# Performance work log

Hardware: AMD Instinct MI355X
Metric: run time of the kernel (lower is better)

Reference implementation:

```python
import jax, jax.numpy as jnp
import numpy as np
from jax import lax

DIM = 256
D_STATE = 16
SPARSITY = 0.3


def setup_inputs() -> dict:
    key = jax.random.key(0)
    ks = jax.random.split(key, 12)
    B, L, C = 16, 8192, DIM
    x = jax.random.normal(ks[0], (B, L, C), dtype=jnp.float32)
    # DyT params
    alpha = jnp.ones((1,), jnp.float32) * 0.5
    dyt_w = jnp.ones((C,), jnp.float32) + 0.02 * jax.random.normal(ks[1], (C,))
    dyt_b = 0.02 * jax.random.normal(ks[2], (C,))
    # proj_in / proj_out (torch Linear: y = x @ W.T + b)
    s = 1.0 / np.sqrt(C)
    Wi = jax.random.uniform(ks[3], (C, C), minval=-s, maxval=s)
    bi = jax.random.uniform(ks[4], (C,), minval=-s, maxval=s)
    Wo = jax.random.uniform(ks[5], (C, C), minval=-s, maxval=s)
    bo = jax.random.uniform(ks[6], (C,), minval=-s, maxval=s)
    # depthwise kernel_size=1 conv -> per-channel scale
    conv_w = jax.random.uniform(ks[7], (C,), minval=-1.0, maxval=1.0)
    # SSM params (nn.Parameter zeros in source; use small random for a meaningful test)
    A = 0.02 * jax.random.normal(ks[8], (D_STATE, D_STATE))
    Bp = 0.02 * jax.random.normal(ks[9], (1, 1, D_STATE))
    Cp = 0.02 * jax.random.normal(ks[10], (C, D_STATE))
    return {"x": x, "alpha": alpha, "dyt_w": dyt_w, "dyt_b": dyt_b,
            "Wi": Wi, "bi": bi, "conv_w": conv_w,
            "A": A, "Bp": Bp, "Cp": Cp, "Wo": Wo, "bo": bo}


def reference(x, alpha, dyt_w, dyt_b, Wi, bi, conv_w, A, Bp, Cp, Wo, bo):
    B, L, C = x.shape
    residual = x
    # DyT norm
    x_norm = jnp.tanh(alpha * x) * dyt_w + dyt_b
    # proj_in
    x_proj = x_norm @ Wi.T + bi                      # [B, L, C]
    # cosine similarity to center token, softmax over L
    center = x_proj[:, L // 2]                        # [B, C]
    eps = 1e-12
    xpn = x_proj / jnp.maximum(jnp.linalg.norm(x_proj, axis=-1, keepdims=True), eps)
    cn = center / jnp.maximum(jnp.linalg.norm(center, axis=-1, keepdims=True), eps)
    sim = jax.nn.softmax(jnp.einsum('blc,bc->bl', xpn, cn), axis=-1)  # [B, L]
    k = max(1, int(L * SPARSITY))
    _, topk_idx = lax.top_k(sim, k)                   # [B, k]
    # gather selected tokens
    x_sparse = jnp.take_along_axis(x_proj, topk_idx[:, :, None], axis=1)  # [B, k, C]
    # depthwise kernel-1 conv == per-channel scale
    x_conv = x_sparse * conv_w                        # [B, k, C]
    # SSM scan: h_{t} = h_{t-1} @ A.T + sigmoid(B) * x_t;  y_t = sum(h * sigmoid(C))
    sB = jax.nn.sigmoid(Bp)                           # [1, 1, d_state]
    sC = jax.nn.sigmoid(Cp)                           # [C, d_state]

    def step(h, xt):
        # h: [B, C, d_state], xt: [B, C]
        h = h @ A.T + sB * xt[:, :, None]
        y = jnp.sum(h * sC, axis=-1)                  # [B, C]
        return h, y

    h0 = jnp.zeros((B, C, D_STATE), x.dtype)
    _, ys = lax.scan(step, h0, jnp.swapaxes(x_conv, 0, 1))  # ys: [k, B, C]
    x_processed = jnp.swapaxes(ys, 0, 1) @ Wo.T + bo        # [B, k, C]
    # scatter back to full sequence (topk indices are unique per row)
    out = jnp.zeros_like(x).at[jnp.arange(B)[:, None], topk_idx].set(x_processed)
    return out + residual, sim
```

## Files before the change

### kernel.cpp

```cpp
#include <hip/hip_runtime.h>
#include <math.h>

#define B_ 16
#define L_ 8192
#define C_ 256
#define KTOP 2457
#define JT 20
#define M1 (B_*L_)
#define M2 (B_*KTOP)

#define XP_OFF  ((size_t)0)
#define Y_OFF   (XP_OFF + (size_t)M1*C_)
#define CN_OFF  (Y_OFF  + (size_t)M2*C_)
#define CF_OFF  (CN_OFF + (size_t)B_*C_)
#define IDX_OFF (CF_OFF + (size_t)JT*C_)
#define WIT_OFF (IDX_OFF + (size_t)M2)
#define WOT_OFF (WIT_OFF + (size_t)C_*C_)

__device__ __forceinline__ void async_copy16(const float* g, float* l) {
    __builtin_amdgcn_global_load_lds(
        (const __attribute__((address_space(1))) void*)g,
        (__attribute__((address_space(3))) void*)l, 16, 0, 0);
}

__global__ __launch_bounds__(256) void prep_kernel(
    const float* __restrict__ Wi, const float* __restrict__ Wo,
    float* __restrict__ WiT, float* __restrict__ WoT,
    const float* __restrict__ A, const float* __restrict__ Bp, const float* __restrict__ Cp,
    float* __restrict__ cf,
    const float* __restrict__ x, const float* __restrict__ bi, const float* __restrict__ alpha,
    const float* __restrict__ dw, const float* __restrict__ db, float* __restrict__ cn)
{
    __shared__ float shm[1089];
    const int bid = blockIdx.x, tid = threadIdx.x;
    if (bid < 128) {
        const int z = bid >> 6, rem = bid & 63;
        const int r0 = (rem >> 3) * 32, c0 = (rem & 7) * 32;
        const float* src = z ? Wo : Wi;
        float* dst = z ? WoT : WiT;
        float (*t)[33] = (float(*)[33])shm;
        int tx = tid & 31, ty = tid >> 5;
        #pragma unroll
        for (int r = 0; r < 4; r++)
            t[ty + r*8][tx] = src[(size_t)(r0 + ty + r*8)*C_ + c0 + tx];
        __syncthreads();
        #pragma unroll
        for (int r = 0; r < 4; r++)
            dst[(size_t)(c0 + ty + r*8)*C_ + r0 + tx] = t[tx][ty + r*8];
    } else if (bid == 128) {
        int c = tid;
        float* As = shm;
        float* v0 = shm + 256;
        As[c] = A[c];
        if (c < 16) v0[c] = 1.0f / (1.0f + expf(-Bp[c]));
        float sC[16];
        #pragma unroll
        for (int i = 0; i < 16; i++) sC[i] = 1.0f / (1.0f + expf(-Cp[c*16 + i]));
        __syncthreads();
        float v[16];
        #pragma unroll
        for (int i = 0; i < 16; i++) v[i] = v0[i];
        for (int j = 0; j < JT; j++) {
            float d = 0.f;
            #pragma unroll
            for (int i = 0; i < 16; i++) d += sC[i] * v[i];
            cf[j*C_ + c] = d;
            float nv[16];
            #pragma unroll
            for (int i = 0; i < 16; i++) {
                float s = 0.f;
                #pragma unroll
                for (int m = 0; m < 16; m++) s += As[i*16 + m] * v[m];
                nv[i] = s;
            }
            #pragma unroll
            for (int i = 0; i < 16; i++) v[i] = nv[i];
        }
    } else {
        int b = bid - 129, c = tid;
        float* xn = shm;
        float* red = shm + 256;
        float al = alpha[0];
        size_t base = ((size_t)b*L_ + L_/2)*C_;
        xn[c] = tanhf(al*x[base + c])*dw[c] + db[c];
        __syncthreads();
        float s = bi[c];
        #pragma unroll 8
        for (int k = 0; k < 256; k++) s = fmaf(xn[k], Wi[(size_t)c*C_ + k], s);
        float ss = s*s;
        #pragma unroll
        for (int off = 32; off; off >>= 1) ss += __shfl_xor(ss, off);
        if ((c & 63) == 0) red[c >> 6] = ss;
        __syncthreads();
        float tot = red[0] + red[1] + red[2] + red[3];
        float inv = 1.0f / fmaxf(sqrtf(tot), 1e-12f);
        cn[b*C_ + c] = s * inv;
    }
}

__global__ __launch_bounds__(256, 2) void gemm1_kernel(
    const float* __restrict__ x, const float* __restrict__ WiT,
    const float* __restrict__ bi, const float* __restrict__ alpha,
    const float* __restrict__ dw, const float* __restrict__ db,
    const float* __restrict__ cn, float* __restrict__ xp, float* __restrict__ e)
{
    __shared__ float As[32*132];
    __shared__ float Bs[32*256];
    const int tid = threadIdx.x;
    const int lane = tid & 63;
    const int wv = tid >> 6;
    const int tn2 = tid & 31;
    const int tm2 = tid >> 5;
    const int m0 = blockIdx.x * 128;
    const int b  = m0 >> 13;
    const float al = alpha[0];

    float acc[16][8];
    #pragma unroll
    for (int i = 0; i < 16; i++)
        #pragma unroll
        for (int j = 0; j < 8; j++) acc[i][j] = 0.f;

    for (int k0 = 0; k0 < C_; k0 += 32) {
        #pragma unroll
        for (int it = 0; it < 8; it++) {
            int br = wv + it*4;
            async_copy16(&WiT[(size_t)(k0 + br)*C_ + lane*4], &Bs[br*256]);
        }
        #pragma unroll
        for (int it = 0; it < 4; it++) {
            int i2 = tid + it*256;
            int ar = i2 >> 3;
            int ak = (i2 & 7) * 4;
            float4 v  = *(const float4*)&x[(size_t)(m0 + ar)*C_ + k0 + ak];
            float4 w4 = *(const float4*)&dw[k0 + ak];
            float4 b4 = *(const float4*)&db[k0 + ak];
            As[(ak+0)*132 + ar] = tanhf(al*v.x)*w4.x + b4.x;
            As[(ak+1)*132 + ar] = tanhf(al*v.y)*w4.y + b4.y;
            As[(ak+2)*132 + ar] = tanhf(al*v.z)*w4.z + b4.z;
            As[(ak+3)*132 + ar] = tanhf(al*v.w)*w4.w + b4.w;
        }
        __syncthreads();
        #pragma unroll 2
        for (int kk = 0; kk < 32; kk++) {
            float a[16];
            *(float4*)&a[0]  = *(const float4*)&As[kk*132 + tm2*16];
            *(float4*)&a[4]  = *(const float4*)&As[kk*132 + tm2*16 + 4];
            *(float4*)&a[8]  = *(const float4*)&As[kk*132 + tm2*16 + 8];
            *(float4*)&a[12] = *(const float4*)&As[kk*132 + tm2*16 + 12];
            float4 b0 = *(const float4*)&Bs[kk*256 + tn2*4];
            float4 b1 = *(const float4*)&Bs[kk*256 + tn2*4 + 128];
            #pragma unroll
            for (int i = 0; i < 16; i++) {
                acc[i][0] = fmaf(a[i], b0.x, acc[i][0]);
                acc[i][1] = fmaf(a[i], b0.y, acc[i][1]);
                acc[i][2] = fmaf(a[i], b0.z, acc[i][2]);
                acc[i][3] = fmaf(a[i], b0.w, acc[i][3]);
                acc[i][4] = fmaf(a[i], b1.x, acc[i][4]);
                acc[i][5] = fmaf(a[i], b1.y, acc[i][5]);
                acc[i][6] = fmaf(a[i], b1.z, acc[i][6]);
                acc[i][7] = fmaf(a[i], b1.w, acc[i][7]);
            }
        }
        __syncthreads();
    }
    float4 bi0 = *(const float4*)&bi[tn2*4];
    float4 bi1 = *(const float4*)&bi[tn2*4 + 128];
    float4 c0  = *(const float4*)&cn[b*C_ + tn2*4];
    float4 c1  = *(const float4*)&cn[b*C_ + tn2*4 + 128];
    #pragma unroll
    for (int i = 0; i < 16; i++) {
        size_t row = m0 + tm2*16 + i;
        float4 o0 = make_float4(acc[i][0]+bi0.x, acc[i][1]+bi0.y, acc[i][2]+bi0.z, acc[i][3]+bi0.w);
        float4 o1 = make_float4(acc[i][4]+bi1.x, acc[i][5]+bi1.y, acc[i][6]+bi1.z, acc[i][7]+bi1.w);
        *(float4*)&xp[row*C_ + tn2*4]       = o0;
        *(float4*)&xp[row*C_ + tn2*4 + 128] = o1;
        float dt = o0.x*c0.x + o0.y*c0.y + o0.z*c0.z + o0.w*c0.w
                 + o1.x*c1.x + o1.y*c1.y + o1.z*c1.z + o1.w*c1.w;
        float ss = o0.x*o0.x + o0.y*o0.y + o0.z*o0.z + o0.w*o0.w
                 + o1.x*o1.x + o1.y*o1.y + o1.z*o1.z + o1.w*o1.w;
        #pragma unroll
        for (int off = 16; off; off >>= 1) {
            dt += __shfl_xor(dt, off);
            ss += __shfl_xor(ss, off);
        }
        if (tn2 == 0) e[row] = dt / fmaxf(sqrtf(ss), 1e-12f);
    }
}

__global__ __launch_bounds__(1024) void softmax_kernel(
    const float* __restrict__ e, float* __restrict__ sim, unsigned long long* __restrict__ kw)
{
    __shared__ float scratch[32];
    const int b = blockIdx.x, tid = threadIdx.x;
    const int lane = tid & 63, wid = tid >> 6;
    const float* eb = e + (size_t)b*L_;
    float ev[8];
    #pragma unroll
    for (int s = 0; s < 8; s++) ev[s] = eb[tid + s*1024];
    float mx = ev[0];
    #pragma unroll
    for (int s = 1; s < 8; s++) mx = fmaxf(mx, ev[s]);
    #pragma unroll
    for (int off = 32; off; off >>= 1) mx = fmaxf(mx, __shfl_xor(mx, off));
    if (lane == 0) scratch[wid] = mx;
    __syncthreads();
    if (tid == 0) {
        float m2 = scratch[0];
        for (int i = 1; i < 16; i++) m2 = fmaxf(m2, scratch[i]);
        scratch[20] = m2;
    }
    __syncthreads();
    mx = scratch[20];
    float pv[8], sum = 0.f;
    #pragma unroll
    for (int s = 0; s < 8; s++) { pv[s] = expf(ev[s] - mx); sum += pv[s]; }
    #pragma unroll
    for (int off = 32; off; off >>= 1) sum += __shfl_xor(sum, off);
    __syncthreads();
    if (lane == 0) scratch[wid] = sum;
    __syncthreads();
    if (tid == 0) {
        float s2 = 0.f;
        for (int i = 0; i < 16; i++) s2 += scratch[i];
        scratch[21] = s2;
    }
    __syncthreads();
    float inv = 1.0f / scratch[21];
    #pragma unroll
    for (int s = 0; s < 8; s++) {
        int l = tid + s*1024;
        float sm = pv[s] * inv;
        sim[(size_t)b*L_ + l] = sm;
        kw[(size_t)b*L_ + l] =
            ((unsigned long long)__float_as_uint(sm) << 32) | (unsigned)(0xFFFFFFFFu - l);
    }
}

__global__ __launch_bounds__(256) void sort1k_kernel(unsigned long long* __restrict__ keys)
{
    __shared__ unsigned long long k[1024];
    size_t base = (size_t)blockIdx.x * 1024;
    int tid = threadIdx.x;
    #pragma unroll
    for (int s = 0; s < 4; s++) k[tid + s*256] = keys[base + tid + s*256];
    __syncthreads();
    for (int ksz = 2; ksz <= 1024; ksz <<= 1) {
        for (int j = ksz >> 1; j > 0; j >>= 1) {
            #pragma unroll
            for (int s = 0; s < 2; s++) {
                int p = tid + s*256;
                int i = ((p & ~(j-1)) << 1) | (p & (j-1));
                int ix = i | j;
                unsigned long long a = k[i], c = k[ix];
                bool desc = ((i & ksz) == 0);
                if (desc ? (a < c) : (a > c)) { k[i] = c; k[ix] = a; }
            }
            __syncthreads();
        }
    }
    #pragma unroll
    for (int s = 0; s < 4; s++) keys[base + tid + s*256] = k[tid + s*256];
}

#define MT 2048
__global__ __launch_bounds__(256) void merge_kernel(
    const unsigned long long* __restrict__ src, unsigned long long* __restrict__ dst, int run)
{
    const size_t tile = blockIdx.x;
    const size_t pairSpan = (size_t)2 * run;
    const size_t p = tile * MT / pairSpan;
    const int o = (int)(tile * MT % pairSpan);
    const unsigned long long* A  = src + p * pairSpan;
    const unsigned long long* Bv = A + run;
    unsigned long long* D = dst + p * pairSpan;

    int q0 = o + threadIdx.x * (MT/256);
    int lo = (q0 > run) ? (q0 - run) : 0;
    int hi = (q0 < run) ? q0 : run;
    while (lo < hi) {
        int mid = (lo + hi) >> 1;
        if (A[mid] >= Bv[q0 - 1 - mid]) lo = mid + 1; else hi = mid;
    }
    int a = lo, bq = q0 - lo;
    #pragma unroll
    for (int q = 0; q < MT/256; q++) {
        unsigned long long va = (a < run) ? A[a] : 0ULL;
        unsigned long long vb = (bq < run) ? Bv[bq] : 0ULL;
        bool takeA = (bq >= run) || ((a < run) && (va > vb));
        D[q0 + q] = takeA ? va : vb;
        if (takeA) a++; else bq++;
    }
}

__global__ __launch_bounds__(256) void merge_top_kernel(
    const unsigned long long* __restrict__ src, int* __restrict__ idxo)
{
    const int tile = blockIdx.x;
    const int p = tile >> 1;
    const int o = (tile & 1) * MT;
    const int run = 4096;
    const unsigned long long* A  = src + (size_t)p * L_;
    const unsigned long long* Bv = A + run;

    int q0 = o + threadIdx.x * (MT/256);
    int lo = (q0 > run) ? (q0 - run) : 0;
    int hi = (q0 < run) ? q0 : run;
    while (lo < hi) {
        int mid = (lo + hi) >> 1;
        if (A[mid] >= Bv[q0 - 1 - mid]) lo = mid + 1; else hi = mid;
    }
    int a = lo, bq = q0 - lo;
    #pragma unroll
    for (int q = 0; q < MT/256; q++) {
        unsigned long long va = (a < run) ? A[a] : 0ULL;
        unsigned long long vb = (bq < run) ? Bv[bq] : 0ULL;
        bool takeA = (bq >= run) || ((a < run) && (va > vb));
        unsigned long long v = takeA ? va : vb;
        if (q0 + q < KTOP)
            idxo[p*KTOP + q0 + q] = (int)(0xFFFFFFFFu - (unsigned)(v & 0xFFFFFFFFu));
        if (takeA) a++; else bq++;
    }
}

#define TT 32
__global__ __launch_bounds__(256) void y_kernel(const float* __restrict__ xp,
    const int* __restrict__ idx, const float* __restrict__ conv_w,
    const float* __restrict__ cf, float* __restrict__ y)
{
    __shared__ float rows[(TT + JT - 1) * C_];
    const int b = blockIdx.y;
    const int t0 = blockIdx.x * TT;
    const int tid = threadIdx.x;
    const int c4 = (tid & 63) * 4;
    const int tg = tid >> 6;
    const int* idxb = idx + b*KTOP;

    for (int s = tid; s < (TT + JT - 1) * 64; s += 256) {
        int r = s >> 6, cq = (s & 63) * 4;
        int gi = t0 - (JT - 1) + r;
        float4 v = make_float4(0.f, 0.f, 0.f, 0.f);
        if (gi >= 0 && gi < KTOP) {
            int l = idxb[gi];
            v = *(const float4*)&xp[((size_t)b*L_ + l)*C_ + cq];
        }
        *(float4*)&rows[r*C_ + cq] = v;
    }
    float4 cfr[JT];
    #pragma unroll
    for (int j = 0; j < JT; j++) cfr[j] = *(const float4*)&cf[j*C_ + c4];
    float4 cw = *(const float4*)&conv_w[c4];
    __syncthreads();

    #pragma unroll
    for (int u = 0; u < TT/4; u++) {
        int tl = tg + u*4;
        int t = t0 + tl;
        if (t < KTOP) {
            float4 acc = make_float4(0.f, 0.f, 0.f, 0.f);
            #pragma unroll
            for (int j = 0; j < JT; j++) {
                const float4 v = *(const float4*)&rows[(tl + JT - 1 - j)*C_ + c4];
                acc.x = fmaf(cfr[j].x, v.x, acc.x);
                acc.y = fmaf(cfr[j].y, v.y, acc.y);
                acc.z = fmaf(cfr[j].z, v.z, acc.z);
                acc.w = fmaf(cfr[j].w, v.w, acc.w);
            }
            acc.x *= cw.x; acc.y *= cw.y; acc.z *= cw.z; acc.w *= cw.w;
            *(float4*)&y[((size_t)b*KTOP + t)*C_ + c4] = acc;
        }
    }
}

__global__ void copy_kernel(const float4* __restrict__ src, float4* __restrict__ dst)
{
    size_t n4 = (size_t)M1*C_/4;
    for (size_t i = (size_t)blockIdx.x*blockDim.x + threadIdx.x; i < n4;
         i += (size_t)gridDim.x*blockDim.x)
        dst[i] = src[i];
}

__global__ __launch_bounds__(256, 2) void gemm2_kernel(
    const float* __restrict__ y, const float* __restrict__ WoT,
    const float* __restrict__ bo, const float* __restrict__ x,
    const int* __restrict__ idx, float* __restrict__ out0)
{
    __shared__ float As[2][32*132];
    __shared__ float Bs[2][32*128];
    const int tid = threadIdx.x;
    const int lane = tid & 63;
    const int wv = tid >> 6;
    const int tm2 = tid >> 4;
    const int tn2 = tid & 15;
    const int m0 = blockIdx.x * 128;
    const int n0 = blockIdx.y * 128;

    float acc[8][8];
    #pragma unroll
    for (int i = 0; i < 8; i++)
        #pragma unroll
        for (int j = 0; j < 8; j++) acc[i][j] = 0.f;

    float4 xa[4];
    #pragma unroll
    for (int it = 0; it < 4; it++) {
        int i2 = tid + it*256;
        int m = m0 + (i2>>3);
        xa[it] = (m < M2) ? *(const float4*)&y[(size_t)m*C_ + ((i2&7)*4)]
                          : make_float4(0.f, 0.f, 0.f, 0.f);
    }
    #pragma unroll
    for (int it = 0; it < 4; it++) {
        int brow = 2*wv + it*8;
        async_copy16(&WoT[(size_t)(brow + (lane>>5))*C_ + n0 + (lane&31)*4],
                     &Bs[0][brow*128]);
    }
    #pragma unroll
    for (int it = 0; it < 4; it++) {
        int i2 = tid + it*256;
        int ar = i2>>3, ak = (i2&7)*4;
        float4 v = xa[it];
        As[0][(ak+0)*132 + ar] = v.x;
        As[0][(ak+1)*132 + ar] = v.y;
        As[0][(ak+2)*132 + ar] = v.z;
        As[0][(ak+3)*132 + ar] = v.w;
    }
    __syncthreads();
    int cur = 0;
    for (int k0 = 0; k0 < C_; k0 += 32) {
        if (k0 + 32 < C_) {
            int nxt = cur ^ 1;
            #pragma unroll
            for (int it = 0; it < 4; it++) {
                int brow = 2*wv + it*8;
                async_copy16(&WoT[(size_t)(k0 + 32 + brow + (lane>>5))*C_ + n0 + (lane&31)*4],
                             &Bs[nxt][brow*128]);
            }
            #pragma unroll
            for (int it = 0; it < 4; it++) {
                int i2 = tid + it*256;
                int m = m0 + (i2>>3);
                xa[it] = (m < M2) ? *(const float4*)&y[(size_t)m*C_ + k0 + 32 + ((i2&7)*4)]
                                  : make_float4(0.f, 0.f, 0.f, 0.f);
            }
        }
        #pragma unroll 2
        for (int kk = 0; kk < 32; kk++) {
            float a[8], bf[8];
            *(float4*)&a[0]  = *(const float4*)&As[cur][kk*132 + tm2*8];
            *(float4*)&a[4]  = *(const float4*)&As[cur][kk*132 + tm2*8 + 4];
            *(float4*)&bf[0] = *(const float4*)&Bs[cur][kk*128 + tn2*4];
            *(float4*)&bf[4] = *(const float4*)&Bs[cur][kk*128 + tn2*4 + 64];
            #pragma unroll
            for (int i = 0; i < 8; i++)
                #pragma unroll
                for (int j = 0; j < 8; j++)
                    acc[i][j] = fmaf(a[i], bf[j], acc[i][j]);
        }
        if (k0 + 32 < C_) {
            int nxt = cur ^ 1;
            #pragma unroll
            for (int it = 0; it < 4; it++) {
                int i2 = tid + it*256;
                int ar = i2>>3, ak = (i2&7)*4;
                float4 v = xa[it];
                As[nxt][(ak+0)*132 + ar] = v.x;
                As[nxt][(ak+1)*132 + ar] = v.y;
                As[nxt][(ak+2)*132 + ar] = v.z;
                As[nxt][(ak+3)*132 + ar] = v.w;
            }
            cur = nxt;
        }
        __syncthreads();
    }
    float4 bo0 = *(const float4*)&bo[n0 + tn2*4];
    float4 bo1 = *(const float4*)&bo[n0 + 64 + tn2*4];
    #pragma unroll
    for (int i = 0; i < 8; i++) {
        int m = m0 + tm2*8 + i;
        if (m < M2) {
            int b = m / KTOP, t = m - b*KTOP;
            int l = idx[b*KTOP + t];
            size_t base = ((size_t)b*L_ + l)*C_;
            float4 x0 = *(const float4*)&x[base + n0 + tn2*4];
            float4 x1 = *(const float4*)&x[base + n0 + 64 + tn2*4];
            float4 o0 = make_float4(acc[i][0]+bo0.x+x0.x, acc[i][1]+bo0.y+x0.y,
                                    acc[i][2]+bo0.z+x0.z, acc[i][3]+bo0.w+x0.w);
            float4 o1 = make_float4(acc[i][4]+bo1.x+x1.x, acc[i][5]+bo1.y+x1.y,
                                    acc[i][6]+bo1.z+x1.z, acc[i][7]+bo1.w+x1.w);
            *(float4*)&out0[base + n0 + tn2*4]      = o0;
            *(float4*)&out0[base + n0 + 64 + tn2*4] = o1;
        }
    }
}

extern "C" void kernel_launch(void* const* d_in, const int* in_sizes, int n_in,
                              void* d_out, int out_size, void* d_ws, size_t ws_size,
                              hipStream_t stream)
{
    const float* x      = (const float*)d_in[0];
    const float* alpha  = (const float*)d_in[1];
    const float* dyt_w  = (const float*)d_in[2];
    const float* dyt_b  = (const float*)d_in[3];
    const float* Wi     = (const float*)d_in[4];
    const float* bi     = (const float*)d_in[5];
    const float* conv_w = (const float*)d_in[6];
    const float* A      = (const float*)d_in[7];
    const float* Bp     = (const float*)d_in[8];
    const float* Cp     = (const float*)d_in[9];
    const float* Wo     = (const float*)d_in[10];
    const float* bo     = (const float*)d_in[11];

    float* ws  = (float*)d_ws;
    float* xp  = ws + XP_OFF;
    float* yb  = ws + Y_OFF;
    float* cn  = ws + CN_OFF;
    float* cf  = ws + CF_OFF;
    int*   idx = (int*)(ws + IDX_OFF);
    float* WiT = ws + WIT_OFF;
    float* WoT = ws + WOT_OFF;
    unsigned long long* kw1 = (unsigned long long*)(ws + Y_OFF);
    unsigned long long* kw2 = kw1 + (size_t)B_*L_;
    float* e = ws + Y_OFF + 524288;

    float* out0 = (float*)d_out;
    float* sim  = out0 + (size_t)M1*C_;

    prep_kernel<<<145, 256, 0, stream>>>(Wi, Wo, WiT, WoT, A, Bp, Cp, cf,
                                         x, bi, alpha, dyt_w, dyt_b, cn);
    gemm1_kernel<<<M1/128, 256, 0, stream>>>(x, WiT, bi, alpha, dyt_w, dyt_b, cn, xp, e);
    softmax_kernel<<<B_, 1024, 0, stream>>>(e, sim, kw1);
    sort1k_kernel<<<B_*L_/1024, 256, 0, stream>>>(kw1);
    merge_kernel<<<B_*L_/MT, 256, 0, stream>>>(kw1, kw2, 1024);
    merge_kernel<<<B_*L_/MT, 256, 0, stream>>>(kw2, kw1, 2048);
    merge_top_kernel<<<B_*2, 256, 0, stream>>>(kw1, idx);
    y_kernel<<<dim3((KTOP + TT - 1)/TT, B_), 256, 0, stream>>>(xp, idx, conv_w, cf, yb);
    copy_kernel<<<2048, 256, 0, stream>>>((const float4*)x, (float4*)out0);
    gemm2_kernel<<<dim3((M2 + 127)/128, 2), 256, 0, stream>>>(yb, WoT, bo, x, idx, out0);
}
```

Before: 459.1 us.

## Double-buffer gemm1 LDS tiles with register prefetch of next K slice

The proj_in GEMM main loop now uses two LDS buffers with a K step of 16 instead of one buffer with a K step of 32. The next slice of Wi is fetched by async copy and the next x values are loaded into registers while the current slice is being computed. The DyT tanh transform is written to the spare buffer after compute, leaving one barrier per iteration. This aims to hide global load latency behind the FMA work, in exchange for more live registers, twice as many iterations and a smaller per-step tile.

```diff
diff --git a/kernel.cpp b/kernel.cpp
--- a/kernel.cpp
+++ b/kernel.cpp
@@ -104,8 +104,8 @@
     const float* __restrict__ dw, const float* __restrict__ db,
     const float* __restrict__ cn, float* __restrict__ xp, float* __restrict__ e)
 {
-    __shared__ float As[32*132];
-    __shared__ float Bs[32*256];
+    __shared__ float As[2][16*132];
+    __shared__ float Bs[2][16*256];
     const int tid = threadIdx.x;
     const int lane = tid & 63;
     const int wv = tid >> 6;
@@ -114,6 +114,8 @@
     const int m0 = blockIdx.x * 128;
     const int b  = m0 >> 13;
     const float al = alpha[0];
+    const int ar = tid >> 2;
+    const int ak = (tid & 3) * 4;
 
     float acc[16][8];
     #pragma unroll
@@ -121,35 +123,45 @@
         #pragma unroll
         for (int j = 0; j < 8; j++) acc[i][j] = 0.f;
 
-    for (int k0 = 0; k0 < C_; k0 += 32) {
-        #pragma unroll
-        for (int it = 0; it < 8; it++) {
-            int br = wv + it*4;
-            async_copy16(&WiT[(size_t)(k0 + br)*C_ + lane*4], &Bs[br*256]);
-        }
-        #pragma unroll
-        for (int it = 0; it < 4; it++) {
-            int i2 = tid + it*256;
-            int ar = i2 >> 3;
-            int ak = (i2 & 7) * 4;
-            float4 v  = *(const float4*)&x[(size_t)(m0 + ar)*C_ + k0 + ak];
-            float4 w4 = *(const float4*)&dw[k0 + ak];
-            float4 b4 = *(const float4*)&db[k0 + ak];
-            As[(ak+0)*132 + ar] = tanhf(al*v.x)*w4.x + b4.x;
-            As[(ak+1)*132 + ar] = tanhf(al*v.y)*w4.y + b4.y;
-            As[(ak+2)*132 + ar] = tanhf(al*v.z)*w4.z + b4.z;
-            As[(ak+3)*132 + ar] = tanhf(al*v.w)*w4.w + b4.w;
-        }
-        __syncthreads();
+    #pragma unroll
+    for (int it = 0; it < 4; it++)
+        async_copy16(&WiT[(size_t)(wv + it*4)*C_ + lane*4], &Bs[0][(wv + it*4)*256]);
+    {
+        float4 w4 = *(const float4*)&dw[ak];
+        float4 b4 = *(const float4*)&db[ak];
+        #pragma unroll
+        for (int it = 0; it < 2; it++) {
+            int r = ar + it*64;
+            float4 v = *(const float4*)&x[(size_t)(m0 + r)*C_ + ak];
+            As[0][(ak+0)*132 + r] = tanhf(al*v.x)*w4.x + b4.x;
+            As[0][(ak+1)*132 + r] = tanhf(al*v.y)*w4.y + b4.y;
+            As[0][(ak+2)*132 + r] = tanhf(al*v.z)*w4.z + b4.z;
+            As[0][(ak+3)*132 + r] = tanhf(al*v.w)*w4.w + b4.w;
+        }
+    }
+    __syncthreads();
+    int cur = 0;
+    for (int t = 0; t < 16; t++) {
+        const int k0 = t * 16;
+        float4 xa0, xa1;
+        if (t < 15) {
+            int nxt = cur ^ 1;
+            #pragma unroll
+            for (int it = 0; it < 4; it++)
+                async_copy16(&WiT[(size_t)(k0 + 16 + wv + it*4)*C_ + lane*4],
+                             &Bs[nxt][(wv + it*4)*256]);
+            xa0 = *(const float4*)&x[(size_t)(m0 + ar)*C_ + k0 + 16 + ak];
+            xa1 = *(const float4*)&x[(size_t)(m0 + ar + 64)*C_ + k0 + 16 + ak];
+        }
         #pragma unroll 2
-        for (int kk = 0; kk < 32; kk++) {
+        for (int kk = 0; kk < 16; kk++) {
             float a[16];
-            *(float4*)&a[0]  = *(const float4*)&As[kk*132 + tm2*16];
-            *(float4*)&a[4]  = *(const float4*)&As[kk*132 + tm2*16 + 4];
-            *(float4*)&a[8]  = *(const float4*)&As[kk*132 + tm2*16 + 8];
-            *(float4*)&a[12] = *(const float4*)&As[kk*132 + tm2*16 + 12];
-            float4 b0 = *(const float4*)&Bs[kk*256 + tn2*4];
-            float4 b1 = *(const float4*)&Bs[kk*256 + tn2*4 + 128];
+            *(float4*)&a[0]  = *(const float4*)&As[cur][kk*132 + tm2*16];
+            *(float4*)&a[4]  = *(const float4*)&As[cur][kk*132 + tm2*16 + 4];
+            *(float4*)&a[8]  = *(const float4*)&As[cur][kk*132 + tm2*16 + 8];
+            *(float4*)&a[12] = *(const float4*)&As[cur][kk*132 + tm2*16 + 12];
+            float4 b0 = *(const float4*)&Bs[cur][kk*256 + tn2*4];
+            float4 b1 = *(const float4*)&Bs[cur][kk*256 + tn2*4 + 128];
             #pragma unroll
             for (int i = 0; i < 16; i++) {
                 acc[i][0] = fmaf(a[i], b0.x, acc[i][0]);
@@ -161,6 +173,20 @@
                 acc[i][6] = fmaf(a[i], b1.z, acc[i][6]);
                 acc[i][7] = fmaf(a[i], b1.w, acc[i][7]);
             }
+        }
+        if (t < 15) {
+            int nxt = cur ^ 1;
+            float4 w4 = *(const float4*)&dw[k0 + 16 + ak];
+            float4 b4 = *(const float4*)&db[k0 + 16 + ak];
+            As[nxt][(ak+0)*132 + ar] = tanhf(al*xa0.x)*w4.x + b4.x;
+            As[nxt][(ak+1)*132 + ar] = tanhf(al*xa0.y)*w4.y + b4.y;
+            As[nxt][(ak+2)*132 + ar] = tanhf(al*xa0.z)*w4.z + b4.z;
+            As[nxt][(ak+3)*132 + ar] = tanhf(al*xa0.w)*w4.w + b4.w;
+            As[nxt][(ak+0)*132 + ar + 64] = tanhf(al*xa1.x)*w4.x + b4.x;
+            As[nxt][(ak+1)*132 + ar + 64] = tanhf(al*xa1.y)*w4.y + b4.y;
+            As[nxt][(ak+2)*132 + ar + 64] = tanhf(al*xa1.z)*w4.z + b4.z;
+            As[nxt][(ak+3)*132 + ar + 64] = tanhf(al*xa1.w)*w4.w + b4.w;
+            cur = nxt;
         }
         __syncthreads();
     }
```

Result: no change. 450.7 us (-1.8%).
